# Performance work log

Hardware: AMD Instinct MI355X
Metric: run time of the kernel (lower is better)

The kernel has to match this reference:

```python
import jax, jax.numpy as jnp
import numpy as np
from jax import lax


def _mdlstm_dir(x, Wx, Wh, Wv, b):
    # x: [H, W, B, Cin]; one diagonal-causal 2D-LSTM scan (top-left origin).
    H, W, B, Cin = x.shape
    C = Wh.shape[0]
    xa = jnp.einsum('hwbi,ic->hwbc', x, Wx) + b  # [H,W,B,5C] precomputed input gates

    def col_step(carry, inp):
        h_l, c_l = carry                    # left neighbor [B,C]
        xa_ij, h_u, c_u = inp               # input preact, up neighbor
        a = xa_ij + h_l @ Wh + h_u @ Wv     # [B,5C]
        i, f1, f2, o, g = jnp.split(a, 5, axis=-1)
        c = jax.nn.sigmoid(i) * jnp.tanh(g) + jax.nn.sigmoid(f1) * c_l + jax.nn.sigmoid(f2) * c_u
        h = jax.nn.sigmoid(o) * jnp.tanh(c)
        return (h, c), (h, c)

    z = jnp.zeros((B, C), x.dtype)
    zrow = jnp.zeros((W, B, C), x.dtype)

    def row_step(carry, xa_row):
        h_up, c_up = carry                  # [W,B,C]
        _, (hs, cs) = lax.scan(col_step, (z, z), (xa_row, h_up, c_up))
        return (hs, cs), hs

    _, hh = lax.scan(row_step, (zrow, zrow), xa)  # [H,W,B,C]
    return hh


def _mdlstm4(x, Wx, Wh, Wv, b):
    # x: [B,Cin,H,W] -> per-direction outputs [4,H,W,B,C] (directions: TL, TR, BL, BR origins)
    xt = jnp.transpose(x, (2, 3, 0, 1))  # [H,W,B,Cin]
    x4 = jnp.stack([xt, xt[:, ::-1], xt[::-1], xt[::-1, ::-1]])
    o = jax.vmap(_mdlstm_dir)(x4, Wx, Wh, Wv, b)  # [4,H,W,B,C]
    return jnp.stack([o[0], o[1][:, ::-1], o[2][::-1], o[3][::-1, ::-1]])


def _block(x, Wx, Wh, Wv, b, cw, cb):
    h4 = _mdlstm4(x, Wx, Wh, Wv, b)            # [4,H,W,B,C]
    h = jnp.transpose(h4.sum(0), (2, 3, 0, 1))  # sum directions -> [B,C,H,W]
    y = lax.conv_general_dilated(h, cw, window_strides=(2, 2), padding='VALID',
                                 dimension_numbers=('NCHW', 'OIHW', 'NCHW'))
    return jnp.tanh(y + cb[None, :, None, None])


def _forward(x, p0_Wx, p0_Wh, p0_Wv, p0_b, c0_w, c0_b,
             p1_Wx, p1_Wh, p1_Wv, p1_b, c1_w, c1_b,
             p2_Wx, p2_Wh, p2_Wv, p2_b, dW, db):
    x = _block(x, p0_Wx, p0_Wh, p0_Wv, p0_b, c0_w, c0_b)  # [B,6,31,126]
    x = _block(x, p1_Wx, p1_Wh, p1_Wv, p1_b, c1_w, c1_b)  # [B,20,14,61]
    h4 = _mdlstm4(x, p2_Wx, p2_Wh, p2_Wv, p2_b)           # [4,H,W,B,50]
    # per-direction Linear(50->100) then sum over the 4 directions
    out = jnp.einsum('dhwbc,dcn->bhwn', h4, dW) + db.sum(0)
    return out  # [B,14,61,100]


def setup_inputs() -> dict:
    key = jax.random.key(0)
    ks = jax.random.split(key, 20)
    rn = lambda k, s, sc=0.1: jax.random.normal(k, s, jnp.float32) * sc
    return {
        'x': jax.random.normal(ks[0], (16, 1, 64, 256), jnp.float32),
        'p0_Wx': rn(ks[1], (4, 1, 10)), 'p0_Wh': rn(ks[2], (4, 2, 10)),
        'p0_Wv': rn(ks[3], (4, 2, 10)), 'p0_b': rn(ks[4], (4, 10)),
        'c0_w': rn(ks[5], (6, 2, 2, 4)), 'c0_b': rn(ks[6], (6,)),
        'p1_Wx': rn(ks[7], (4, 6, 50)), 'p1_Wh': rn(ks[8], (4, 10, 50)),
        'p1_Wv': rn(ks[9], (4, 10, 50)), 'p1_b': rn(ks[10], (4, 50)),
        'c1_w': rn(ks[11], (20, 10, 2, 4)), 'c1_b': rn(ks[12], (20,)),
        'p2_Wx': rn(ks[13], (4, 20, 250)), 'p2_Wh': rn(ks[14], (4, 50, 250)),
        'p2_Wv': rn(ks[15], (4, 50, 250)), 'p2_b': rn(ks[16], (4, 250)),
        'dW': rn(ks[17], (4, 50, 100)), 'db': rn(ks[18], (4, 100)),
    }


def reference(x, p0_Wx, p0_Wh, p0_Wv, p0_b, c0_w, c0_b,
              p1_Wx, p1_Wh, p1_Wv, p1_b, c1_w, c1_b,
              p2_Wx, p2_Wh, p2_Wv, p2_b, dW, db):
    return _forward(x, p0_Wx, p0_Wh, p0_Wv, p0_b, c0_w, c0_b,
                    p1_Wx, p1_Wh, p1_Wv, p1_b, c1_w, c1_b,
                    p2_Wx, p2_Wh, p2_Wv, p2_b, dW, db)
```

## Files before the change

kernel.cpp:

```cpp
#include <hip/hip_runtime.h>

typedef unsigned short ushort_t;
typedef __attribute__((ext_vector_type(8))) short short8;
typedef __attribute__((ext_vector_type(4))) float float4_t;
typedef __attribute__((ext_vector_type(2))) float v2f;

__device__ __forceinline__ float frcp(float x) { return __builtin_amdgcn_rcpf(x); }
__device__ __forceinline__ float fsig(float x) { return frcp(1.f + __expf(-x)); }
__device__ __forceinline__ float ftanh(float x) { return 1.f - 2.f * frcp(1.f + __expf(2.f * x)); }
__device__ __forceinline__ float sig_e2(float a) { return frcp(1.f + __builtin_amdgcn_exp2f(a)); }
__device__ __forceinline__ float th_e2(float a) { return 1.f - 2.f * frcp(1.f + __builtin_amdgcn_exp2f(a)); }

__device__ __forceinline__ ushort_t f2bf(float f) {
    union { float f; unsigned u; } v; v.f = f;
    unsigned u = v.u;
    unsigned r = (u + 0x7fffu + ((u >> 16) & 1u)) >> 16;
    return (ushort_t)r;
}
__device__ __forceinline__ float bf2f(ushort_t s) {
    union { unsigned u; float f; } v; v.u = ((unsigned)s) << 16;
    return v.f;
}
__device__ __forceinline__ float dpp_shr1(float x) {
    int i = __builtin_bit_cast(int, x);
    int r = __builtin_amdgcn_update_dpp(0, i, 0x138 , 0xf, 0xf, true);
    return __builtin_bit_cast(float, r);
}

__global__ __launch_bounds__(64) void k_mdlstm0(
    const float* __restrict__ x, const float* __restrict__ Wx,
    const float* __restrict__ Wh, const float* __restrict__ Wv,
    const float* __restrict__ bias, float* __restrict__ h0)
{
    const int dir = blockIdx.x >> 4, b = blockIdx.x & 15;
    const int lane = threadIdx.x;
    const bool fH = dir >= 2, fW = (dir & 1) != 0;
    const int ri = fH ? 63 - lane : lane;
    const float L2E = 1.44269504088896340736f;

    __shared__ float Xs[64 * 256];
    {
        const float* xg = x + b * 64 * 256;
        for (int i4 = lane; i4 < 4096; i4 += 64) {
            int row = i4 >> 6, c4 = (i4 & 63) << 2;
            float4 v = *(const float4*)(xg + (row << 8) + c4);
            *(float4*)&Xs[(row << 8) + c4] = v;
        }
    }
    __syncthreads();

    v2f wx[5], bs[5], wh0[5], wh1[5], wv0[5], wv1[5];
#pragma unroll
    for (int g = 0; g < 5; g++) {
        float sc = (g == 4) ? 2.f * L2E : -L2E;
#pragma unroll
        for (int un = 0; un < 2; un++) {
            int n = g * 2 + un;
            wx[g][un]  = Wx[dir * 10 + n] * sc;
            bs[g][un]  = bias[dir * 10 + n] * sc;
            wh0[g][un] = Wh[(dir * 2 + 0) * 10 + n] * sc;
            wh1[g][un] = Wh[(dir * 2 + 1) * 10 + n] * sc;
            wv0[g][un] = Wv[(dir * 2 + 0) * 10 + n] * sc;
            wv1[g][un] = Wv[(dir * 2 + 1) * 10 + n] * sc;
        }
    }

    float* orow = h0 + (((dir * 16 + b) * 64 + ri) * 256) * 2;
    v2f hB = {0.f, 0.f}, cB = {0.f, 0.f};

    auto ldx = [&](int j) -> float {
        int jc = j < 0 ? 0 : (j > 255 ? 255 : j);
        int cj = fW ? 255 - jc : jc;
        return Xs[(ri << 8) + cj];
    };
    auto cellf = [&](float xv, v2f hl, v2f cl, float hu0, float hu1,
                     float cu0, float cu1, v2f& hn, v2f& cn) {
        v2f a[5];
#pragma unroll
        for (int g = 0; g < 5; g++) {
            v2f t = __builtin_elementwise_fma((v2f){xv, xv}, wx[g], bs[g]);
            t = __builtin_elementwise_fma((v2f){hl.x, hl.x}, wh0[g], t);
            t = __builtin_elementwise_fma((v2f){hl.y, hl.y}, wh1[g], t);
            t = __builtin_elementwise_fma((v2f){hu0, hu0}, wv0[g], t);
            t = __builtin_elementwise_fma((v2f){hu1, hu1}, wv1[g], t);
            a[g] = t;
        }
        v2f si  = {sig_e2(a[0].x), sig_e2(a[0].y)};
        v2f sf1 = {sig_e2(a[1].x), sig_e2(a[1].y)};
        v2f sf2 = {sig_e2(a[2].x), sig_e2(a[2].y)};
        v2f so  = {sig_e2(a[3].x), sig_e2(a[3].y)};
        v2f tg  = {th_e2(a[4].x),  th_e2(a[4].y)};
        v2f cu  = {cu0, cu1};
        cn = si * tg + sf1 * cl + sf2 * cu;
        v2f tc = {th_e2(cn.x * (2.f * L2E)), th_e2(cn.y * (2.f * L2E))};
        hn = so * tc;
    };

    float xA0 = ldx(0 - lane), xB0 = ldx(1 - lane);
    float xA1 = ldx(2 - lane), xB1 = ldx(3 - lane);

    for (int t = 0; t < 160; t++) {
        const int jA = 2 * t - lane, jB = jA + 1;
        float xA = xA0, xB = xB0;
        xA0 = xA1; xB0 = xB1;
        xA1 = ldx(2 * (t + 2) - lane); xB1 = ldx(2 * (t + 2) + 1 - lane);

        float huA0 = dpp_shr1(hB.x), huA1 = dpp_shr1(hB.y);
        float cuA0 = dpp_shr1(cB.x), cuA1 = dpp_shr1(cB.y);
        v2f hA, cA;
        cellf(xA, hB, cB, huA0, huA1, cuA0, cuA1, hA, cA);
        bool actA = (jA >= 0) && (jA < 256);
        if (!actA) { hA = (v2f){0.f, 0.f}; cA = (v2f){0.f, 0.f}; }

        float huB0 = dpp_shr1(hA.x), huB1 = dpp_shr1(hA.y);
        float cuB0 = dpp_shr1(cA.x), cuB1 = dpp_shr1(cA.y);
        v2f hN, cN;
        cellf(xB, hA, cA, huB0, huB1, cuB0, cuB1, hN, cN);
        bool actB = (jB >= 0) && (jB < 256);
        if (!actB) { hN = (v2f){0.f, 0.f}; cN = (v2f){0.f, 0.f}; }
        hB = hN; cB = cN;

        if (actA) {
            int cj = fW ? 255 - jA : jA;
            float2 hv; hv.x = hA.x; hv.y = hA.y;
            *(float2*)&orow[cj * 2] = hv;
        }
        if (actB) {
            int cj = fW ? 255 - jB : jB;
            float2 hv; hv.x = hB.x; hv.y = hB.y;
            *(float2*)&orow[cj * 2] = hv;
        }
    }
}

__global__ __launch_bounds__(128) void k_conv0(
    const float* __restrict__ h0, const float* __restrict__ cw,
    const float* __restrict__ cb, float* __restrict__ x1)
{
    int blk = blockIdx.x;
    int oh = blk / 127, ow = blk % 127;
    int t = threadIdx.x;
    if (t >= 96) return;
    int b = t / 6, co = t % 6;
    float w[2][2][4];
#pragma unroll
    for (int ci = 0; ci < 2; ci++)
#pragma unroll
        for (int kh = 0; kh < 2; kh++)
#pragma unroll
            for (int kw = 0; kw < 4; kw++)
                w[ci][kh][kw] = cw[((co * 2 + ci) * 2 + kh) * 4 + kw];
    float acc = cb[co];
    for (int dirb = 0; dirb < 4; dirb++) {
#pragma unroll
        for (int kh = 0; kh < 2; kh++) {
#pragma unroll
            for (int kw = 0; kw < 4; kw++) {
                const float* ptr = h0 + ((((dirb * 16 + b) * 64) + (2 * oh + kh)) * 256 + (2 * ow + kw)) * 2;
                float2 hv = *(const float2*)ptr;
                acc = fmaf(hv.x, w[0][kh][kw], acc);
                acc = fmaf(hv.y, w[1][kh][kw], acc);
            }
        }
    }
    x1[((oh * 127 + ow) * 16 + b) * 6 + co] = ftanh(acc);
}

__global__ __launch_bounds__(320, 1) void k_mdlstm1(
    const float* __restrict__ x1, const float* __restrict__ Wx,
    const float* __restrict__ Wh, const float* __restrict__ Wv,
    const float* __restrict__ bias, float* __restrict__ h1)
{
    const int dir = blockIdx.x >> 4, b = blockIdx.x & 15;
    const bool fH = dir >= 2, fW = (dir & 1) != 0;
    const int tid = threadIdx.x;
    const int wave = tid >> 6, lane = tid & 63;

    __shared__ float Xs1[32 * 127 * 6];
    __shared__ __align__(16) ushort_t Ah[2][32][40];
    __shared__ __align__(16) ushort_t Al[2][32][40];
    __shared__ float P[32][68];
    __shared__ float cbuf[2][33][12];

    for (int i = tid; i < 2 * 32 * 40; i += 320) { ((ushort_t*)Ah)[i] = 0; ((ushort_t*)Al)[i] = 0; }
    for (int i = tid; i < 2 * 33 * 12; i += 320) ((float*)cbuf)[i] = 0.f;
    for (int i = tid; i < 32 * 127 * 6; i += 320)
        Xs1[i] = x1[(i / 6) * 96 + b * 6 + (i % 6)];
    __syncthreads();
    if (tid < 6) {
        int rr = fH ? 31 : 0, cc = fW ? 126 : 0;
        float xv = Xs1[(rr * 127 + cc) * 6 + tid];
        ushort_t xh = f2bf(xv);
        Ah[0][0][20 + tid] = xh;
        Al[0][0][20 + tid] = f2bf(xv - bf2f(xh));
    }

    const int mt = wave & 1, nt0 = (wave >> 1) * 2;
    short8 bh0 = {0,0,0,0,0,0,0,0}, bl0 = {0,0,0,0,0,0,0,0};
    short8 bh1 = {0,0,0,0,0,0,0,0}, bl1 = {0,0,0,0,0,0,0,0};
    if (wave < 4) {
#pragma unroll
        for (int t = 0; t < 2; t++) {
            int n = (nt0 + t) * 16 + (lane & 15);
#pragma unroll
            for (int jj = 0; jj < 8; jj++) {
                int k = (lane >> 4) * 8 + jj;
                float v = 0.f;
                if (n < 50) {
                    if (k < 10)      v = Wh[(dir * 10 + k) * 50 + n];
                    else if (k < 20) v = Wv[(dir * 10 + (k - 10)) * 50 + n];
                    else if (k < 26) v = Wx[(dir * 6 + (k - 20)) * 50 + n];
                }
                ushort_t hi = f2bf(v);
                ushort_t lo = f2bf(v - bf2f(hi));
                if (t == 0) { bh0[jj] = (short)hi; bl0[jj] = (short)lo; }
                else        { bh1[jj] = (short)hi; bl1[jj] = (short)lo; }
            }
        }
    }

    const int cell = tid / 10, u = tid % 10;
    float br[5];
#pragma unroll
    for (int g = 0; g < 5; g++) br[g] = bias[dir * 50 + g * 10 + u];
    const int ri = fH ? 31 - cell : cell;
    float creg = 0.f;
    __syncthreads();

    int p = 0;
    for (int d = 0; d < 158; d++) {
        if (wave < 4) {
            const int arow = mt * 16 + (lane & 15);
            const int koff = (lane >> 4) * 8;
            short8 ah = *(const short8*)&Ah[p][arow][koff];
            short8 al = *(const short8*)&Al[p][arow][koff];
            float4_t acc0 = {0.f, 0.f, 0.f, 0.f};
            float4_t acc1 = {0.f, 0.f, 0.f, 0.f};
            acc0 = __builtin_amdgcn_mfma_f32_16x16x32_bf16(ah, bh0, acc0, 0, 0, 0);
            acc1 = __builtin_amdgcn_mfma_f32_16x16x32_bf16(ah, bh1, acc1, 0, 0, 0);
            acc0 = __builtin_amdgcn_mfma_f32_16x16x32_bf16(al, bh0, acc0, 0, 0, 0);
            acc1 = __builtin_amdgcn_mfma_f32_16x16x32_bf16(al, bh1, acc1, 0, 0, 0);
            acc0 = __builtin_amdgcn_mfma_f32_16x16x32_bf16(ah, bl0, acc0, 0, 0, 0);
            acc1 = __builtin_amdgcn_mfma_f32_16x16x32_bf16(ah, bl1, acc1, 0, 0, 0);
            int col0 = nt0 * 16 + (lane & 15);
            int r0 = (lane >> 4) * 4;
#pragma unroll
            for (int r = 0; r < 4; r++) P[mt * 16 + r0 + r][col0] = acc0[r];
#pragma unroll
            for (int r = 0; r < 4; r++) P[mt * 16 + r0 + r][col0 + 16] = acc1[r];
        } else {
#pragma unroll
            for (int it = 0; it < 3; it++) {
                int item = lane + it * 64;
                int xc = item / 6, ci = item % 6;
                int jn = d + 1 - xc;
                if (jn >= 0 && jn < 127) {
                    int rr = fH ? 31 - xc : xc, cc = fW ? 126 - jn : jn;
                    float xv = Xs1[(rr * 127 + cc) * 6 + ci];
                    ushort_t xh = f2bf(xv);
                    Ah[1 - p][xc][20 + ci] = xh;
                    Al[1 - p][xc][20 + ci] = f2bf(xv - bf2f(xh));
                }
            }
        }
        __syncthreads();

        {
            int j = d - cell;
            if (j >= 0 && j < 127) {
                float ai  = P[cell][u]      + br[0];
                float af1 = P[cell][10 + u] + br[1];
                float af2 = P[cell][20 + u] + br[2];
                float ao  = P[cell][30 + u] + br[3];
                float ag  = P[cell][40 + u] + br[4];
                float cu = cbuf[p][cell][u];
                float cn = fsig(ai) * ftanh(ag) + fsig(af1) * creg + fsig(af2) * cu;
                float hn = fsig(ao) * ftanh(cn);
                creg = cn;
                cbuf[1 - p][cell + 1][u] = cn;
                ushort_t hh = f2bf(hn);
                float hhf = bf2f(hh);
                ushort_t hlo = f2bf(hn - hhf);
                Ah[1 - p][cell][u] = hh;
                Al[1 - p][cell][u] = hlo;
                if (cell < 31) { Ah[1 - p][cell + 1][10 + u] = hh; Al[1 - p][cell + 1][10 + u] = hlo; }
                int cj = fW ? 126 - j : j;
                h1[(((dir * 16 + b) * 32 + ri) * 127 + cj) * 10 + u] = hn;
            }
        }
        __syncthreads();
        p ^= 1;
    }
}

__global__ __launch_bounds__(320, 1) void k_conv1(
    const float* __restrict__ h1, const float* __restrict__ cw,
    const float* __restrict__ cb, float* __restrict__ x2)
{
    int blk = blockIdx.x;
    int oh = blk / 62, ow = blk % 62;
    int t = threadIdx.x;
    int b = t / 20, co = t % 20;
    float w[10][2][4];
#pragma unroll
    for (int ci = 0; ci < 10; ci++)
#pragma unroll
        for (int kh = 0; kh < 2; kh++)
#pragma unroll
            for (int kw = 0; kw < 4; kw++)
                w[ci][kh][kw] = cw[((co * 10 + ci) * 2 + kh) * 4 + kw];
    float acc = cb[co];
    for (int dirb = 0; dirb < 4; dirb++) {
#pragma unroll
        for (int kh = 0; kh < 2; kh++) {
#pragma unroll
            for (int kw = 0; kw < 4; kw++) {
                const float* ptr = h1 + ((((dirb * 16 + b) * 32) + (2 * oh + kh)) * 127 + (2 * ow + kw)) * 10;
#pragma unroll
                for (int ci = 0; ci < 10; ci++)
                    acc = fmaf(ptr[ci], w[ci][kh][kw], acc);
            }
        }
    }
    x2[((oh * 62 + ow) * 16 + b) * 20 + co] = ftanh(acc);
}

__global__ __launch_bounds__(256) void k_prepB2(
    const float* __restrict__ Wh, const float* __restrict__ Wv,
    const float* __restrict__ Wx, ushort_t* __restrict__ Bh,
    ushort_t* __restrict__ Bl)
{
    int idx = blockIdx.x * 256 + threadIdx.x;
    if (idx >= 131072) return;
    int dir = idx >> 15; int k = (idx >> 8) & 127; int n = idx & 255;
    float v = 0.f;
    if (n < 250) {
        if (k < 50)       v = Wh[(dir * 50 + k) * 250 + n];
        else if (k < 100) v = Wv[(dir * 50 + (k - 50)) * 250 + n];
        else if (k < 120) v = Wx[(dir * 20 + (k - 100)) * 250 + n];
    }
    ushort_t hi = f2bf(v);
    Bh[idx] = hi;
    Bl[idx] = f2bf(v - bf2f(hi));
}

__global__ __launch_bounds__(1024, 1) void k_mdlstm2(
    const float* __restrict__ x2, const ushort_t* __restrict__ BmH,
    const ushort_t* __restrict__ BmL,
    const float* __restrict__ bias, float* __restrict__ h2)
{
    const int dir = blockIdx.x >> 4, b = blockIdx.x & 15;
    const bool fH = dir >= 2, fW = (dir & 1) != 0;
    const int tid = threadIdx.x;
    const int wave = tid >> 6, lane = tid & 63;

    __shared__ float Xs2[16 * 62 * 20];
    __shared__ __align__(16) ushort_t Ah[2][16][136];
    __shared__ __align__(16) ushort_t Al[2][16][136];
    __shared__ float P[16][260];
    __shared__ float cbuf[2][16][52];

    for (int i = tid; i < 2 * 16 * 136; i += 1024) { ((ushort_t*)Ah)[i] = 0; ((ushort_t*)Al)[i] = 0; }
    for (int i = tid; i < 16 * 62 * 20; i += 1024)
        Xs2[i] = x2[(i / 20) * 320 + b * 20 + (i % 20)];
    __syncthreads();
    if (tid < 20) {
        int ci = tid;
        int rr = fH ? 15 : 0, cc = fW ? 61 : 0;
        float xv = Xs2[(rr * 62 + cc) * 20 + ci];
        ushort_t xh = f2bf(xv);
        Ah[0][0][100 + ci] = xh;
        Al[0][0][100 + ci] = f2bf(xv - bf2f(xh));
    }

    short8 bfragH[4], bfragL[4];
    {
        const int n = wave * 16 + (lane & 15);
#pragma unroll
        for (int q = 0; q < 4; q++) {
#pragma unroll
            for (int jj = 0; jj < 8; jj++) {
                int k = q * 32 + (lane >> 4) * 8 + jj;
                bfragH[q][jj] = (short)BmH[(dir * 128 + k) * 256 + n];
                bfragL[q][jj] = (short)BmL[(dir * 128 + k) * 256 + n];
            }
        }
    }

    const int cell = tid / 50, u = tid % 50;
    float bi = 0, bf1 = 0, bf2v = 0, bo = 0, bg = 0;
    if (tid < 800) {
        bi   = bias[dir * 250 + u];
        bf1  = bias[dir * 250 + 50 + u];
        bf2v = bias[dir * 250 + 100 + u];
        bo   = bias[dir * 250 + 150 + u];
        bg   = bias[dir * 250 + 200 + u];
    }
    const int rr_c = fH ? 15 - cell : cell;
    float creg = 0.f;
    __syncthreads();

    int p = 0;
    for (int d = 0; d < 77; d++) {
        {
            const int arow = lane & 15;
            const int koff = (lane >> 4) * 8;
            short8 ah[4], al[4];
#pragma unroll
            for (int q = 0; q < 4; q++) {
                ah[q] = *(const short8*)&Ah[p][arow][q * 32 + koff];
                al[q] = *(const short8*)&Al[p][arow][q * 32 + koff];
            }
            float4_t acc = {0.f, 0.f, 0.f, 0.f};
#pragma unroll
            for (int q = 0; q < 4; q++) acc = __builtin_amdgcn_mfma_f32_16x16x32_bf16(ah[q], bfragH[q], acc, 0, 0, 0);
#pragma unroll
            for (int q = 0; q < 4; q++) acc = __builtin_amdgcn_mfma_f32_16x16x32_bf16(al[q], bfragH[q], acc, 0, 0, 0);
#pragma unroll
            for (int q = 0; q < 4; q++) acc = __builtin_amdgcn_mfma_f32_16x16x32_bf16(ah[q], bfragL[q], acc, 0, 0, 0);
            int col = wave * 16 + (lane & 15);
            int r0 = (lane >> 4) * 4;
#pragma unroll
            for (int r = 0; r < 4; r++) P[r0 + r][col] = acc[r];
        }
        __syncthreads();

        if (tid < 800) {
            int j = d - cell;
            if (j >= 0 && j < 62) {
                float ai  = P[cell][u] + bi;
                float af1 = P[cell][50 + u] + bf1;
                float af2 = P[cell][100 + u] + bf2v;
                float ao  = P[cell][150 + u] + bo;
                float ag  = P[cell][200 + u] + bg;
                float cu = (cell == 0) ? 0.f : cbuf[p][cell - 1][u];
                float cn = fsig(ai) * ftanh(ag) + fsig(af1) * creg + fsig(af2) * cu;
                float hn = fsig(ao) * ftanh(cn);
                creg = cn;
                cbuf[1 - p][cell][u] = cn;
                ushort_t hh = f2bf(hn);
                float hhf = bf2f(hh);
                ushort_t hlo = f2bf(hn - hhf);
                Ah[1 - p][cell][u] = hh;
                Al[1 - p][cell][u] = hlo;
                if (cell < 15) { Ah[1 - p][cell + 1][50 + u] = hh; Al[1 - p][cell + 1][50 + u] = hlo; }
                int cc = fW ? 61 - j : j;
                h2[(((dir * 16 + b) * 16 + rr_c) * 62 + cc) * 50 + u] = hn;
            }
        } else if (tid >= 832 && tid < 992) {
            int s = tid - 832;
#pragma unroll
            for (int it = 0; it < 2; it++) {
                int item = s + it * 160;
                int xc = item / 20, ci = item % 20;
                int jn = d + 1 - xc;
                if (jn >= 0 && jn < 62) {
                    int rr = fH ? 15 - xc : xc, cc = fW ? 61 - jn : jn;
                    float xv = Xs2[(rr * 62 + cc) * 20 + ci];
                    ushort_t xh = f2bf(xv);
                    Ah[1 - p][xc][100 + ci] = xh;
                    Al[1 - p][xc][100 + ci] = f2bf(xv - bf2f(xh));
                }
            }
        }
        __syncthreads();
        p ^= 1;
    }
}

__global__ __launch_bounds__(256) void k_final(
    const float* __restrict__ h2, const float* __restrict__ dW,
    const float* __restrict__ db, float* __restrict__ out)
{
    int blk = blockIdx.x;
    int r = blk / 62, c = blk % 62;
    int t = threadIdx.x;
    __shared__ float hb[3200];
    for (int i = t; i < 3200; i += 256) {
        int dirb = i / 800, rem = i % 800, b = rem / 50, u = rem % 50;
        hb[i] = h2[(((dirb * 16 + b) * 16 + r) * 62 + c) * 50 + u];
    }
    __syncthreads();
    for (int o = t; o < 1600; o += 256) {
        int b = o / 100, n = o % 100;
        float acc = db[n] + db[100 + n] + db[200 + n] + db[300 + n];
#pragma unroll
        for (int dirb = 0; dirb < 4; dirb++) {
            const float* hp = hb + (dirb * 16 + b) * 50;
            const float* wp = dW + dirb * 5000 + n;
#pragma unroll 10
            for (int cc2 = 0; cc2 < 50; cc2++)
                acc = fmaf(hp[cc2], wp[cc2 * 100], acc);
        }
        out[((b * 16 + r) * 62 + c) * 100 + n] = acc;
    }
}

extern "C" void kernel_launch(void* const* d_in, const int* in_sizes, int n_in,
                              void* d_out, int out_size, void* d_ws, size_t ws_size,
                              hipStream_t stream)
{
    const float* x     = (const float*)d_in[0];
    const float* p0_Wx = (const float*)d_in[1];
    const float* p0_Wh = (const float*)d_in[2];
    const float* p0_Wv = (const float*)d_in[3];
    const float* p0_b  = (const float*)d_in[4];
    const float* c0_w  = (const float*)d_in[5];
    const float* c0_b  = (const float*)d_in[6];
    const float* p1_Wx = (const float*)d_in[7];
    const float* p1_Wh = (const float*)d_in[8];
    const float* p1_Wv = (const float*)d_in[9];
    const float* p1_b  = (const float*)d_in[10];
    const float* c1_w  = (const float*)d_in[11];
    const float* c1_b  = (const float*)d_in[12];
    const float* p2_Wx = (const float*)d_in[13];
    const float* p2_Wh = (const float*)d_in[14];
    const float* p2_Wv = (const float*)d_in[15];
    const float* p2_b  = (const float*)d_in[16];
    const float* dW    = (const float*)d_in[17];
    const float* db    = (const float*)d_in[18];
    float* out = (float*)d_out;
    float* ws  = (float*)d_ws;

    float* h0 = ws;
    float* x1 = h0 + 2097152;
    float* h1 = x1 + 390144;
    float* x2 = h1 + 2600960;
    float* h2 = x2 + 317440;
    ushort_t* BmH = (ushort_t*)(h2 + 3174400);
    ushort_t* BmL = BmH + 131072;

    k_prepB2<<<512, 256, 0, stream>>>(p2_Wh, p2_Wv, p2_Wx, BmH, BmL);
    k_mdlstm0<<<64, 64, 0, stream>>>(x, p0_Wx, p0_Wh, p0_Wv, p0_b, h0);
    k_conv0<<<32 * 127, 128, 0, stream>>>(h0, c0_w, c0_b, x1);
    k_mdlstm1<<<64, 320, 0, stream>>>(x1, p1_Wx, p1_Wh, p1_Wv, p1_b, h1);
    k_conv1<<<16 * 62, 320, 0, stream>>>(h1, c1_w, c1_b, x2);
    k_mdlstm2<<<64, 1024, 0, stream>>>(x2, BmH, BmL, p2_b, h2);
    k_final<<<16 * 62, 256, 0, stream>>>(h2, dW, db, out);
}
```

Before: 494.2 us.

## Restructure layer-1 MDLSTM kernel into two self-contained waves with one barrier per step

The layer-1 MDLSTM kernel drops from 320 threads (four MFMA waves, one input-loading wave, cell work spread across all threads) to 128 threads in two waves. Each wave owns 16 rows and handles its own MFMA gate products over all four n-tiles, writes them to a private transposed LDS buffer, runs the LSTM cell updates for its 160 (row, unit) items at three per lane, and stages the next input column. Because the gate buffer is read only by the wave that wrote it, the barrier between the matmul and the cell update goes away, leaving one block barrier per diagonal step. The cost is more serial MFMA and transcendental work per wave on a latency-bound recurrence, and fewer waves to hide that latency.

```diff
diff --git a/kernel.cpp b/kernel.cpp
--- a/kernel.cpp
+++ b/kernel.cpp
@@ -166,7 +166,7 @@
     x1[((oh * 127 + ow) * 16 + b) * 6 + co] = ftanh(acc);
 }
 
-__global__ __launch_bounds__(320, 1) void k_mdlstm1(
+__global__ __launch_bounds__(128, 1) void k_mdlstm1(
     const float* __restrict__ x1, const float* __restrict__ Wx,
     const float* __restrict__ Wh, const float* __restrict__ Wv,
     const float* __restrict__ bias, float* __restrict__ h1)
@@ -179,12 +179,12 @@
     __shared__ float Xs1[32 * 127 * 6];
     __shared__ __align__(16) ushort_t Ah[2][32][40];
     __shared__ __align__(16) ushort_t Al[2][32][40];
-    __shared__ float P[32][68];
+    __shared__ __align__(16) float Pb[2][1040];
     __shared__ float cbuf[2][33][12];
 
-    for (int i = tid; i < 2 * 32 * 40; i += 320) { ((ushort_t*)Ah)[i] = 0; ((ushort_t*)Al)[i] = 0; }
-    for (int i = tid; i < 2 * 33 * 12; i += 320) ((float*)cbuf)[i] = 0.f;
-    for (int i = tid; i < 32 * 127 * 6; i += 320)
+    for (int i = tid; i < 2 * 32 * 40; i += 128) { ((ushort_t*)Ah)[i] = 0; ((ushort_t*)Al)[i] = 0; }
+    for (int i = tid; i < 2 * 33 * 12; i += 128) ((float*)cbuf)[i] = 0.f;
+    for (int i = tid; i < 32 * 127 * 6; i += 128)
         Xs1[i] = x1[(i / 6) * 96 + b * 6 + (i % 6)];
     __syncthreads();
     if (tid < 6) {
@@ -195,97 +195,108 @@
         Al[0][0][20 + tid] = f2bf(xv - bf2f(xh));
     }
 
-    const int mt = wave & 1, nt0 = (wave >> 1) * 2;
-    short8 bh0 = {0,0,0,0,0,0,0,0}, bl0 = {0,0,0,0,0,0,0,0};
-    short8 bh1 = {0,0,0,0,0,0,0,0}, bl1 = {0,0,0,0,0,0,0,0};
-    if (wave < 4) {
-#pragma unroll
-        for (int t = 0; t < 2; t++) {
-            int n = (nt0 + t) * 16 + (lane & 15);
-#pragma unroll
-            for (int jj = 0; jj < 8; jj++) {
-                int k = (lane >> 4) * 8 + jj;
-                float v = 0.f;
-                if (n < 50) {
-                    if (k < 10)      v = Wh[(dir * 10 + k) * 50 + n];
-                    else if (k < 20) v = Wv[(dir * 10 + (k - 10)) * 50 + n];
-                    else if (k < 26) v = Wx[(dir * 6 + (k - 20)) * 50 + n];
-                }
-                ushort_t hi = f2bf(v);
-                ushort_t lo = f2bf(v - bf2f(hi));
-                if (t == 0) { bh0[jj] = (short)hi; bl0[jj] = (short)lo; }
-                else        { bh1[jj] = (short)hi; bl1[jj] = (short)lo; }
-            }
-        }
-    }
-
-    const int cell = tid / 10, u = tid % 10;
-    float br[5];
-#pragma unroll
-    for (int g = 0; g < 5; g++) br[g] = bias[dir * 50 + g * 10 + u];
-    const int ri = fH ? 31 - cell : cell;
-    float creg = 0.f;
+    short8 bh[4], bl[4];
+#pragma unroll
+    for (int nt = 0; nt < 4; nt++) {
+        int n = nt * 16 + (lane & 15);
+#pragma unroll
+        for (int jj = 0; jj < 8; jj++) {
+            int k = (lane >> 4) * 8 + jj;
+            float v = 0.f;
+            if (n < 50) {
+                if (k < 10)      v = Wh[(dir * 10 + k) * 50 + n];
+                else if (k < 20) v = Wv[(dir * 10 + (k - 10)) * 50 + n];
+                else if (k < 26) v = Wx[(dir * 6 + (k - 20)) * 50 + n];
+            }
+            ushort_t hi = f2bf(v);
+            bh[nt][jj] = (short)hi;
+            bl[nt][jj] = (short)f2bf(v - bf2f(hi));
+        }
+    }
+
+    int pcell[3], pu[3];
+    bool pval[3];
+    float br[3][5];
+    float creg[3] = {0.f, 0.f, 0.f};
+#pragma unroll
+    for (int k2 = 0; k2 < 3; k2++) {
+        int idx = lane + 64 * k2;
+        pval[k2] = idx < 160;
+        int cl = (idx < 160) ? idx / 10 : 0;
+        int u  = idx % 10;
+        pcell[k2] = cl; pu[k2] = u;
+#pragma unroll
+        for (int g = 0; g < 5; g++) br[k2][g] = bias[dir * 50 + g * 10 + u];
+    }
     __syncthreads();
 
     int p = 0;
     for (int d = 0; d < 158; d++) {
-        if (wave < 4) {
-            const int arow = mt * 16 + (lane & 15);
+        {
+            const int arow = wave * 16 + (lane & 15);
             const int koff = (lane >> 4) * 8;
             short8 ah = *(const short8*)&Ah[p][arow][koff];
             short8 al = *(const short8*)&Al[p][arow][koff];
-            float4_t acc0 = {0.f, 0.f, 0.f, 0.f};
-            float4_t acc1 = {0.f, 0.f, 0.f, 0.f};
-            acc0 = __builtin_amdgcn_mfma_f32_16x16x32_bf16(ah, bh0, acc0, 0, 0, 0);
-            acc1 = __builtin_amdgcn_mfma_f32_16x16x32_bf16(ah, bh1, acc1, 0, 0, 0);
-            acc0 = __builtin_amdgcn_mfma_f32_16x16x32_bf16(al, bh0, acc0, 0, 0, 0);
-            acc1 = __builtin_amdgcn_mfma_f32_16x16x32_bf16(al, bh1, acc1, 0, 0, 0);
-            acc0 = __builtin_amdgcn_mfma_f32_16x16x32_bf16(ah, bl0, acc0, 0, 0, 0);
-            acc1 = __builtin_amdgcn_mfma_f32_16x16x32_bf16(ah, bl1, acc1, 0, 0, 0);
-            int col0 = nt0 * 16 + (lane & 15);
-            int r0 = (lane >> 4) * 4;
-#pragma unroll
-            for (int r = 0; r < 4; r++) P[mt * 16 + r0 + r][col0] = acc0[r];
-#pragma unroll
-            for (int r = 0; r < 4; r++) P[mt * 16 + r0 + r][col0 + 16] = acc1[r];
-        } else {
-#pragma unroll
-            for (int it = 0; it < 3; it++) {
-                int item = lane + it * 64;
-                int xc = item / 6, ci = item % 6;
-                int jn = d + 1 - xc;
-                if (jn >= 0 && jn < 127) {
-                    int rr = fH ? 31 - xc : xc, cc = fW ? 126 - jn : jn;
-                    float xv = Xs1[(rr * 127 + cc) * 6 + ci];
-                    ushort_t xh = f2bf(xv);
-                    Ah[1 - p][xc][20 + ci] = xh;
-                    Al[1 - p][xc][20 + ci] = f2bf(xv - bf2f(xh));
-                }
-            }
-        }
-        __syncthreads();
-
-        {
-            int j = d - cell;
+            float4_t acc[4];
+#pragma unroll
+            for (int nt = 0; nt < 4; nt++) {
+                float4_t a0 = {0.f, 0.f, 0.f, 0.f};
+                a0 = __builtin_amdgcn_mfma_f32_16x16x32_bf16(ah, bh[nt], a0, 0, 0, 0);
+                a0 = __builtin_amdgcn_mfma_f32_16x16x32_bf16(al, bh[nt], a0, 0, 0, 0);
+                a0 = __builtin_amdgcn_mfma_f32_16x16x32_bf16(ah, bl[nt], a0, 0, 0, 0);
+                acc[nt] = a0;
+            }
+            int colb = lane & 15, quad = lane >> 4;
+#pragma unroll
+            for (int nt = 0; nt < 4; nt++) {
+                int c2 = nt * 16 + colb;
+                if (c2 < 50) *(float4_t*)&Pb[wave][c2 * 20 + quad * 4] = acc[nt];
+            }
+        }
+
+#pragma unroll
+        for (int k2 = 0; k2 < 3; k2++) {
+            if (!pval[k2]) continue;
+            int cl = pcell[k2], u = pu[k2];
+            int gcell = wave * 16 + cl;
+            int j = d - gcell;
             if (j >= 0 && j < 127) {
-                float ai  = P[cell][u]      + br[0];
-                float af1 = P[cell][10 + u] + br[1];
-                float af2 = P[cell][20 + u] + br[2];
-                float ao  = P[cell][30 + u] + br[3];
-                float ag  = P[cell][40 + u] + br[4];
-                float cu = cbuf[p][cell][u];
-                float cn = fsig(ai) * ftanh(ag) + fsig(af1) * creg + fsig(af2) * cu;
+                float ai  = Pb[wave][(u)      * 20 + cl] + br[k2][0];
+                float af1 = Pb[wave][(10 + u) * 20 + cl] + br[k2][1];
+                float af2 = Pb[wave][(20 + u) * 20 + cl] + br[k2][2];
+                float ao  = Pb[wave][(30 + u) * 20 + cl] + br[k2][3];
+                float ag  = Pb[wave][(40 + u) * 20 + cl] + br[k2][4];
+                float cu = cbuf[p][gcell][u];
+                float cn = fsig(ai) * ftanh(ag) + fsig(af1) * creg[k2] + fsig(af2) * cu;
                 float hn = fsig(ao) * ftanh(cn);
-                creg = cn;
-                cbuf[1 - p][cell + 1][u] = cn;
+                creg[k2] = cn;
+                cbuf[1 - p][gcell + 1][u] = cn;
                 ushort_t hh = f2bf(hn);
                 float hhf = bf2f(hh);
                 ushort_t hlo = f2bf(hn - hhf);
-                Ah[1 - p][cell][u] = hh;
-                Al[1 - p][cell][u] = hlo;
-                if (cell < 31) { Ah[1 - p][cell + 1][10 + u] = hh; Al[1 - p][cell + 1][10 + u] = hlo; }
+                Ah[1 - p][gcell][u] = hh;
+                Al[1 - p][gcell][u] = hlo;
+                if (gcell < 31) { Ah[1 - p][gcell + 1][10 + u] = hh; Al[1 - p][gcell + 1][10 + u] = hlo; }
+                int ri = fH ? 31 - gcell : gcell;
                 int cj = fW ? 126 - j : j;
                 h1[(((dir * 16 + b) * 32 + ri) * 127 + cj) * 10 + u] = hn;
+            }
+        }
+
+#pragma unroll
+        for (int it = 0; it < 2; it++) {
+            int item = lane + it * 64;
+            if (item < 96) {
+                int rloc = item / 6, ci = item % 6;
+                int gx = wave * 16 + rloc;
+                int jn = d + 1 - gx;
+                if (jn >= 0 && jn < 127) {
+                    int rr = fH ? 31 - gx : gx, cc = fW ? 126 - jn : jn;
+                    float xv = Xs1[(rr * 127 + cc) * 6 + ci];
+                    ushort_t xh = f2bf(xv);
+                    Ah[1 - p][gx][20 + ci] = xh;
+                    Al[1 - p][gx][20 + ci] = f2bf(xv - bf2f(xh));
+                }
             }
         }
         __syncthreads();
@@ -533,7 +544,7 @@
     k_prepB2<<<512, 256, 0, stream>>>(p2_Wh, p2_Wv, p2_Wx, BmH, BmL);
     k_mdlstm0<<<64, 64, 0, stream>>>(x, p0_Wx, p0_Wh, p0_Wv, p0_b, h0);
     k_conv0<<<32 * 127, 128, 0, stream>>>(h0, c0_w, c0_b, x1);
-    k_mdlstm1<<<64, 320, 0, stream>>>(x1, p1_Wx, p1_Wh, p1_Wv, p1_b, h1);
+    k_mdlstm1<<<64, 128, 0, stream>>>(x1, p1_Wx, p1_Wh, p1_Wv, p1_b, h1);
     k_conv1<<<16 * 62, 320, 0, stream>>>(h1, c1_w, c1_b, x2);
     k_mdlstm2<<<64, 1024, 0, stream>>>(x2, BmH, BmL, p2_b, h2);
     k_final<<<16 * 62, 256, 0, stream>>>(h2, dW, db, out);
```

Measured after the change: 561.7 us. 13.7% more time.
